# Performance work log

Measured on AMD Instinct MI355X. Metric: run time of the kernel, lower is better.

## Reference

```python
import jax, jax.numpy as jnp
import numpy as np

N_REL = 8


def setup_inputs() -> dict:
    key = jax.random.key(0)
    ks = jax.random.split(key, 16)
    N, E = 100_000, 1_600_000
    rn = lambda k, shape, s=0.1: jax.random.normal(k, shape, dtype=jnp.float32) * s
    return {
        "x": rn(ks[0], (N, 3), 1.0),
        "edge_index": jax.random.randint(ks[1], (2, E), 0, N),
        "edge_attr": rn(ks[2], (E, 2), 1.0),
        "edge_type": jax.random.randint(ks[3], (E,), 0, N_REL),
        "omega": rn(ks[4], (N, 2), 1.0),
        # encoder weights
        "Wn": rn(ks[5], (3, 64)), "bn": jnp.zeros((64,), jnp.float32),
        "We": rn(ks[6], (2, 32)), "be": jnp.zeros((32,), jnp.float32),
        "Wo": rn(ks[7], (2, 64)), "bo": jnp.zeros((64,), jnp.float32),
        # RGCN layer 1 (edge-feature-aware): per-relation W over concat(x_src, e) -> 64
        "W1": rn(ks[8], (N_REL, 96, 64)), "Wroot1": rn(ks[9], (64, 64)), "b1": jnp.zeros((64,), jnp.float32),
        # RGCN layer 2 (PyG RGCNConv, aggr='max')
        "W2": rn(ks[10], (N_REL, 64, 64)), "Wroot2": rn(ks[11], (64, 64)), "b2": jnp.zeros((64,), jnp.float32),
        # head
        "Wagg": rn(ks[12], (128, 64)), "bagg": jnp.zeros((64,), jnp.float32),
        "Wc": rn(ks[13], (64, 1)), "bc": jnp.zeros((1,), jnp.float32),
    }


def reference(x, edge_index, edge_attr, edge_type, omega,
              Wn, bn, We, be, Wo, bo,
              W1, Wroot1, b1, W2, Wroot2, b2,
              Wagg, bagg, Wc, bc):
    N = x.shape[0]
    n = jax.nn.relu(x @ Wn + bn)            # [N,64]
    e = jax.nn.relu(edge_attr @ We + be)    # [E,32]
    o = jax.nn.relu(omega @ Wo + bo)        # [N,64]
    src, dst = edge_index[0], edge_index[1]

    # --- RGCN layer 1: per-relation transform of [x_src || e], sum-aggregate ---
    feat = jnp.concatenate([n[src], e], axis=1)  # [E,96]
    acc = n @ Wroot1 + b1                        # root/self term
    for r in range(N_REL):
        m = (edge_type == r).astype(feat.dtype)[:, None]
        acc = acc + jax.ops.segment_sum((feat * m) @ W1[r], dst, num_segments=N)
    h = jax.nn.relu(acc)                         # [N,64]

    # --- RGCN layer 2: per-relation transform of x_src, max-aggregate per relation, sum over relations ---
    hs = h[src]                                  # [E,64]
    neg = jnp.finfo(h.dtype).min
    acc2 = h @ Wroot2 + b2
    for r in range(N_REL):
        mask = (edge_type == r)[:, None]
        msg = jnp.where(mask, hs @ W2[r], neg)
        mx = jax.ops.segment_max(msg, dst, num_segments=N)
        acc2 = acc2 + jnp.where(mx > neg * 0.5, mx, 0.0)  # empty segments -> 0 (PyG zeros-init scatter)
    h2 = jax.nn.relu(acc2)                       # [N,64]

    out = jax.nn.relu(jnp.concatenate([h2, o], axis=1) @ Wagg + bagg)
    return jnp.tanh(out @ Wc + bc) * 5.0
```

## Files before the change

### kernel.cpp

```cpp
#include <hip/hip_runtime.h>
#include <cmath>

typedef __attribute__((ext_vector_type(8))) short short8;
typedef __attribute__((ext_vector_type(4))) float floatx4;

__device__ __forceinline__ unsigned short rnbf(float f) {
    unsigned u = __float_as_uint(f);
    u += 0x7fffu + ((u >> 16) & 1u);
    return (unsigned short)(u >> 16);
}
__device__ __forceinline__ float bf2f(unsigned short h) {
    return __uint_as_float(((unsigned)h) << 16);
}
__device__ __forceinline__ int rfl(int v) { return __builtin_amdgcn_readfirstlane(v); }
__device__ __forceinline__ float eAct(unsigned ry, float we0, float we1, float bev) {
    float a0 = __uint_as_float(ry & 0xFFFF0000u);
    float a1 = __uint_as_float(ry << 16);
    return fmaxf(fmaf(a1, we1, fmaf(a0, we0, bev)), 0.f);
}
__device__ __forceinline__ unsigned vidx(int x, unsigned pl, int lane) {
    return (((unsigned)x >> 24) & 7u)*pl + (unsigned)(x & 0xFFFFFF)*64u + (unsigned)lane;
}
__device__ __forceinline__ void mstep(int r, float v, int& cur, float& mx, float& add) {
    bool nb = (r != cur);
    add += nb ? mx : 0.f;
    mx = nb ? v : fmaxf(mx, v);
    cur = r;
}

__global__ void k_histd(const int* __restrict__ ei, const int* __restrict__ et,
                        int* __restrict__ deg8, int E)
{
    int e = blockIdx.x*blockDim.x + threadIdx.x;
    if (e < E) atomicAdd(&deg8[ei[E + e]*8 + et[e]], 1);
}
#define SCHUNK 1024
__global__ void k_bsum(const int* __restrict__ deg, int* __restrict__ bsum, int K)
{
    __shared__ int s[256];
    int b = blockIdx.x, t = threadIdx.x;
    int base = b*SCHUNK;
    int v = 0;
    for (int k = t; k < SCHUNK; k += 256) { int i = base + k; v += (i < K) ? deg[i] : 0; }
    s[t] = v; __syncthreads();
    for (int o = 128; o; o >>= 1) { if (t < o) s[t] += s[t+o]; __syncthreads(); }
    if (t == 0) bsum[b] = s[0];
}
__global__ void k_bscan(int* __restrict__ bsum, int nb)
{
    __shared__ int ts[256];
    int t = threadIdx.x;
    int v[4]; int loc = 0;
    #pragma unroll
    for (int u = 0; u < 4; ++u) { int i = t*4+u; v[u] = (i < nb) ? bsum[i] : 0; loc += v[u]; }
    ts[t] = loc; __syncthreads();
    for (int o = 1; o < 256; o <<= 1) {
        int add = (t >= o) ? ts[t-o] : 0;
        __syncthreads();
        ts[t] += add;
        __syncthreads();
    }
    int excl = ts[t] - loc;
    #pragma unroll
    for (int u = 0; u < 4; ++u) {
        int i = t*4+u;
        if (i < nb) bsum[i] = excl;
        excl += v[u];
    }
}
__global__ void k_bapply(const int* __restrict__ deg, const int* __restrict__ bsum,
                         int* __restrict__ off, int* __restrict__ cursor, int K)
{
    __shared__ int ts[256];
    int b = blockIdx.x, t = threadIdx.x;
    int base = b*SCHUNK;
    int v[4]; int loc = 0;
    #pragma unroll
    for (int u = 0; u < 4; ++u) { int i = base + t*4 + u; v[u] = (i < K) ? deg[i] : 0; loc += v[u]; }
    ts[t] = loc; __syncthreads();
    for (int o = 1; o < 256; o <<= 1) {
        int add = (t >= o) ? ts[t-o] : 0;
        __syncthreads();
        ts[t] += add;
        __syncthreads();
    }
    int excl = ts[t] - loc + bsum[b];
    #pragma unroll
    for (int u = 0; u < 4; ++u) {
        int i = base + t*4 + u;
        if (i < K) { off[i] = excl; cursor[i] = excl; }
        excl += v[u];
        if (i == K-1) off[K] = excl;
    }
}
__global__ void k_scatd(const int* __restrict__ ei, const float* __restrict__ ea,
                        const int* __restrict__ et, int* __restrict__ cursor,
                        int2* __restrict__ srec, int E)
{
    int e = blockIdx.x*blockDim.x + threadIdx.x;
    if (e >= E) return;
    int rel = et[e];
    int key = ei[E + e]*8 + rel;
    int pos = atomicAdd(&cursor[key], 1);
    float2 a = ((const float2*)ea)[e];
    int xv = ei[e] | (rel << 24);
    int yv = ((int)rnbf(a.x) << 16) | (int)rnbf(a.y);
    srec[pos] = make_int2(xv, yv);
}

#define PB_KEYS 4096
#define PA_CH   4096
__global__ __launch_bounds__(256) void k_cnt256(
    const int* __restrict__ ei, int* __restrict__ bktCnt, int E, int nbkt)
{
    __shared__ int cnt[512];
    for (int j = threadIdx.x; j < nbkt; j += 256) cnt[j] = 0;
    __syncthreads();
    int stride = gridDim.x*256;
    for (int e = blockIdx.x*256 + threadIdx.x; e < E; e += stride)
        atomicAdd(&cnt[ei[E + e] >> 9], 1);
    __syncthreads();
    for (int j = threadIdx.x; j < nbkt; j += 256) {
        int c = cnt[j];
        if (c) atomicAdd(&bktCnt[j], c);
    }
}
__global__ void k_scan256(const int* __restrict__ bktCnt, int* __restrict__ bktBase,
                          int* __restrict__ bktCur, int nbkt)
{
    __shared__ int ts[256];
    int t = threadIdx.x;
    int v = (t < nbkt) ? bktCnt[t] : 0;
    ts[t] = v; __syncthreads();
    for (int o = 1; o < 256; o <<= 1) {
        int add = (t >= o) ? ts[t-o] : 0;
        __syncthreads();
        ts[t] += add;
        __syncthreads();
    }
    int excl = ts[t] - v;
    if (t < nbkt) { bktBase[t] = excl; bktCur[t] = excl; }
    if (t == nbkt - 1) bktBase[nbkt] = excl + v;
}
__global__ __launch_bounds__(256) void k_partA(
    const int* __restrict__ ei, const float* __restrict__ ea,
    const int* __restrict__ et, int* __restrict__ bktCur,
    int2* __restrict__ tmp, int E, int nbkt)
{
    __shared__ int cnt[512], base[512];
    int b0 = blockIdx.x * PA_CH;
    for (int j = threadIdx.x; j < nbkt; j += 256) cnt[j] = 0;
    __syncthreads();
    int2 rec[16]; int bk[16];
    #pragma unroll
    for (int u = 0; u < 16; ++u) {
        int e = b0 + u*256 + threadIdx.x;
        bk[u] = -1;
        if (e < E) {
            int rel = et[e];
            int src = ei[e];
            int dst = ei[E + e];
            float2 a = ((const float2*)ea)[e];
            rec[u] = make_int2(src | (rel << 17) | ((dst & 511) << 20),
                               ((int)rnbf(a.x) << 16) | (int)rnbf(a.y));
            bk[u] = dst >> 9;
            atomicAdd(&cnt[bk[u]], 1);
        }
    }
    __syncthreads();
    for (int j = threadIdx.x; j < nbkt; j += 256) {
        int c = cnt[j];
        base[j] = c ? atomicAdd(&bktCur[j], c) : 0;
    }
    __syncthreads();
    for (int j = threadIdx.x; j < nbkt; j += 256) cnt[j] = 0;
    __syncthreads();
    #pragma unroll
    for (int u = 0; u < 16; ++u) {
        if (bk[u] >= 0) {
            int pos = base[bk[u]] + atomicAdd(&cnt[bk[u]], 1);
            tmp[pos] = rec[u];
        }
    }
}
__global__ __launch_bounds__(256) void k_partB2(
    const int2* __restrict__ tmp, const int* __restrict__ bktBase,
    int* __restrict__ off8, int2* __restrict__ srec, int K8)
{
    __shared__ int cnt[PB_KEYS];
    __shared__ int ts[256];
    int b = blockIdx.x;
    int kbase = b * PB_KEYS;
    int kend = kbase + PB_KEYS; if (kend > K8) kend = K8;
    int nk = kend - kbase;
    int bstart = bktBase[b];
    int bend = bktBase[b + 1];
    int t = threadIdx.x;
    for (int j = t; j < PB_KEYS; j += 256) cnt[j] = 0;
    __syncthreads();
    for (int i = bstart + t; i < bend; i += 256) {
        unsigned xw = (unsigned)tmp[i].x;
        int key = (int)((xw >> 20) & 511u)*8 + (int)((xw >> 17) & 7u);
        atomicAdd(&cnt[key], 1);
    }
    __syncthreads();
    int loc[16]; int lsum = 0;
    #pragma unroll
    for (int u = 0; u < 16; ++u) { loc[u] = cnt[t*16 + u]; lsum += loc[u]; }
    ts[t] = lsum; __syncthreads();
    for (int o = 1; o < 256; o <<= 1) {
        int add = (t >= o) ? ts[t-o] : 0;
        __syncthreads();
        ts[t] += add;
        __syncthreads();
    }
    int excl = ts[t] - lsum + bstart;
    #pragma unroll
    for (int u = 0; u < 16; ++u) {
        int j = t*16 + u;
        cnt[j] = excl;
        if (j < nk) off8[kbase + j] = excl;
        excl += loc[u];
    }
    if (t == 0 && kend == K8) off8[K8] = bend;
    __syncthreads();
    for (int i = bstart + t; i < bend; i += 256) {
        int2 r = tmp[i];
        unsigned xw = (unsigned)r.x;
        int src = (int)(xw & 0x1FFFFu);
        int rel = (int)((xw >> 17) & 7u);
        int key = (int)((xw >> 20) & 511u)*8 + rel;
        int pos = atomicAdd(&cnt[key], 1);
        srec[pos] = make_int2(src | (rel << 24), r.y);
    }
}

__global__ __launch_bounds__(64) void k_wpack(
    const float* __restrict__ W1, const float* __restrict__ W2,
    const float* __restrict__ Wroot1, const float* __restrict__ Wroot2,
    const float* __restrict__ Wagg, unsigned short* __restrict__ wpk)
{
    int unit = blockIdx.x >> 2;
    int jt = blockIdx.x & 3;
    int lane = threadIdx.x;
    const float* Wb;
    int kbase;
    if (unit < 16) {
        Wb = W1 + (size_t)(unit >> 1)*96*64;
        kbase = (unit & 1)*32;
    } else if (unit < 32) {
        Wb = W2 + (size_t)((unit - 16) >> 1)*64*64;
        kbase = ((unit - 16) & 1)*32;
    } else if (unit < 40) {
        Wb = W1 + (size_t)(unit - 32)*96*64;
        kbase = 64;
    } else if (unit < 42) {
        Wb = Wroot1; kbase = (unit - 40)*32;
    } else if (unit < 44) {
        Wb = Wroot2; kbase = (unit - 42)*32;
    } else {
        Wb = Wagg;   kbase = (unit - 44)*32;
    }
    int j = jt*16 + (lane & 15);
    size_t base = (((size_t)unit*4 + jt)*64 + lane)*16;
    #pragma unroll
    for (int i = 0; i < 8; ++i) {
        int k = kbase + (lane >> 4)*8 + i;
        float f = Wb[(size_t)k*64 + j];
        unsigned short hi = rnbf(f);
        unsigned short lo = rnbf(f - bf2f(hi));
        wpk[base + i] = hi;
        wpk[base + 8 + i] = lo;
    }
}

__global__ __launch_bounds__(256) void k_encV(
    const float* __restrict__ x,
    const float* __restrict__ Wn, const float* __restrict__ bn,
    const unsigned short* __restrict__ wpk, const float* __restrict__ b1,
    float* __restrict__ acc1, unsigned short* __restrict__ Vbf,
    size_t plane, int N)
{
    int lane = threadIdx.x & 63;
    int wave = threadIdx.x >> 6;
    int n0 = blockIdx.x*64 + 16*wave;
    int m = lane & 15, q = lane >> 4;
    int node = n0 + m; if (node >= N) node = N - 1;
    float x0 = x[3*node], x1 = x[3*node+1], x2 = x[3*node+2];
    short8 ah[2], al[2];
    #pragma unroll
    for (int ks = 0; ks < 2; ++ks) {
        #pragma unroll
        for (int i = 0; i < 8; ++i) {
            int f = ks*32 + q*8 + i;
            float nf = fmaxf(fmaf(x2, Wn[128+f], fmaf(x1, Wn[64+f], fmaf(x0, Wn[f], bn[f]))), 0.f);
            unsigned short hb = rnbf(nf);
            ah[ks][i] = (short)hb;
            al[ks][i] = (short)rnbf(nf - bf2f(hb));
        }
    }
    {
        floatx4 acc[4];
        #pragma unroll
        for (int jt = 0; jt < 4; ++jt) acc[jt] = (floatx4){0.f,0.f,0.f,0.f};
        #pragma unroll
        for (int ks = 0; ks < 2; ++ks) {
            int unit = 40 + ks;
            #pragma unroll
            for (int jt = 0; jt < 4; ++jt) {
                const unsigned short* qp = wpk + (((size_t)unit*4 + jt)*64 + lane)*16;
                short8 bh = *(const short8*)qp;
                short8 bl = *(const short8*)(qp + 8);
                acc[jt] = __builtin_amdgcn_mfma_f32_16x16x32_bf16(ah[ks], bh, acc[jt], 0,0,0);
                acc[jt] = __builtin_amdgcn_mfma_f32_16x16x32_bf16(ah[ks], bl, acc[jt], 0,0,0);
                acc[jt] = __builtin_amdgcn_mfma_f32_16x16x32_bf16(al[ks], bh, acc[jt], 0,0,0);
            }
        }
        #pragma unroll
        for (int jt = 0; jt < 4; ++jt) {
            float bb = b1[jt*16 + m];
            #pragma unroll
            for (int t = 0; t < 4; ++t) {
                int row = n0 + q*4 + t;
                if (row < N) acc1[(size_t)row*64 + jt*16 + m] = acc[jt][t] + bb;
            }
        }
    }
    for (int p = 0; p < 8; ++p) {
        floatx4 acc[4];
        #pragma unroll
        for (int jt = 0; jt < 4; ++jt) acc[jt] = (floatx4){0.f,0.f,0.f,0.f};
        #pragma unroll
        for (int ks = 0; ks < 2; ++ks) {
            int unit = p*2 + ks;
            #pragma unroll
            for (int jt = 0; jt < 4; ++jt) {
                const unsigned short* qp = wpk + (((size_t)unit*4 + jt)*64 + lane)*16;
                short8 bh = *(const short8*)qp;
                short8 bl = *(const short8*)(qp + 8);
                acc[jt] = __builtin_amdgcn_mfma_f32_16x16x32_bf16(ah[ks], bh, acc[jt], 0,0,0);
                acc[jt] = __builtin_amdgcn_mfma_f32_16x16x32_bf16(ah[ks], bl, acc[jt], 0,0,0);
                acc[jt] = __builtin_amdgcn_mfma_f32_16x16x32_bf16(al[ks], bh, acc[jt], 0,0,0);
            }
        }
        unsigned short* Vp = Vbf + (size_t)p*plane;
        #pragma unroll
        for (int jt = 0; jt < 4; ++jt) {
            #pragma unroll
            for (int t = 0; t < 4; ++t) {
                int row = n0 + q*4 + t;
                if (row < N) Vp[(size_t)row*64 + jt*16 + m] = rnbf(acc[jt][t]);
            }
        }
    }
}

__global__ __launch_bounds__(256) void k_encB(
    const float* __restrict__ x,
    const float* __restrict__ Wn, const float* __restrict__ bn,
    const unsigned short* __restrict__ wpk, const float* __restrict__ b1,
    float* __restrict__ nbuf, float* __restrict__ acc1, int N)
{
    int lane = threadIdx.x & 63;
    int wave = threadIdx.x >> 6;
    int n0 = blockIdx.x*64 + 16*wave;
    int m = lane & 15, q = lane >> 4;
    #pragma unroll 4
    for (int t = 0; t < 16; ++t) {
        int nd = n0 + t;
        if (nd < N) {
            float x0 = x[3*nd], x1 = x[3*nd+1], x2 = x[3*nd+2];
            float nj = fmaxf(fmaf(x2, Wn[128+lane], fmaf(x1, Wn[64+lane], fmaf(x0, Wn[lane], bn[lane]))), 0.f);
            nbuf[(size_t)nd*64 + lane] = nj;
        }
    }
    int node = n0 + m; if (node >= N) node = N - 1;
    float x0 = x[3*node], x1 = x[3*node+1], x2 = x[3*node+2];
    short8 ah[2], al[2];
    #pragma unroll
    for (int ks = 0; ks < 2; ++ks) {
        #pragma unroll
        for (int i = 0; i < 8; ++i) {
            int f = ks*32 + q*8 + i;
            float nf = fmaxf(fmaf(x2, Wn[128+f], fmaf(x1, Wn[64+f], fmaf(x0, Wn[f], bn[f]))), 0.f);
            unsigned short hb = rnbf(nf);
            ah[ks][i] = (short)hb;
            al[ks][i] = (short)rnbf(nf - bf2f(hb));
        }
    }
    floatx4 acc[4];
    #pragma unroll
    for (int jt = 0; jt < 4; ++jt) acc[jt] = (floatx4){0.f,0.f,0.f,0.f};
    #pragma unroll
    for (int ks = 0; ks < 2; ++ks) {
        int unit = 40 + ks;
        #pragma unroll
        for (int jt = 0; jt < 4; ++jt) {
            const unsigned short* qp = wpk + (((size_t)unit*4 + jt)*64 + lane)*16;
            short8 bh = *(const short8*)qp;
            short8 bl = *(const short8*)(qp + 8);
            acc[jt] = __builtin_amdgcn_mfma_f32_16x16x32_bf16(ah[ks], bh, acc[jt], 0,0,0);
            acc[jt] = __builtin_amdgcn_mfma_f32_16x16x32_bf16(ah[ks], bl, acc[jt], 0,0,0);
            acc[jt] = __builtin_amdgcn_mfma_f32_16x16x32_bf16(al[ks], bh, acc[jt], 0,0,0);
        }
    }
    #pragma unroll
    for (int jt = 0; jt < 4; ++jt) {
        float bb = b1[jt*16 + m];
        #pragma unroll
        for (int t = 0; t < 4; ++t) {
            int row = n0 + q*4 + t;
            if (row < N) acc1[(size_t)row*64 + jt*16 + m] = acc[jt][t] + bb;
        }
    }
}

__global__ __launch_bounds__(256) void k_vgemmB(
    const float* __restrict__ F, const unsigned short* __restrict__ wpk,
    int unitBase, int g0, int Gc, unsigned short* __restrict__ Vbf,
    size_t plane, int N)
{
    int lane = threadIdx.x & 63;
    int wave = threadIdx.x >> 6;
    int n0 = blockIdx.x*64 + 16*wave;
    int m = lane & 15, q = lane >> 4;
    int node = n0 + m;
    if (node >= N) node = N - 1;
    const float4* Fr = (const float4*)(F + (size_t)node*64);
    short8 ah[2], al[2];
    #pragma unroll
    for (int ks = 0; ks < 2; ++ks) {
        float4 u0 = Fr[ks*8 + q*2];
        float4 u1 = Fr[ks*8 + q*2 + 1];
        float fv[8] = {u0.x,u0.y,u0.z,u0.w,u1.x,u1.y,u1.z,u1.w};
        #pragma unroll
        for (int i = 0; i < 8; ++i) {
            unsigned short hb = rnbf(fv[i]);
            ah[ks][i] = (short)hb;
            al[ks][i] = (short)rnbf(fv[i] - bf2f(hb));
        }
    }
    for (int p = 0; p < Gc; ++p) {
        int rel = g0 + p;
        floatx4 acc[4];
        #pragma unroll
        for (int jt = 0; jt < 4; ++jt) acc[jt] = (floatx4){0.f,0.f,0.f,0.f};
        #pragma unroll
        for (int ks = 0; ks < 2; ++ks) {
            int unit = unitBase + rel*2 + ks;
            #pragma unroll
            for (int jt = 0; jt < 4; ++jt) {
                const unsigned short* qp = wpk + (((size_t)unit*4 + jt)*64 + lane)*16;
                short8 bh = *(const short8*)qp;
                short8 bl = *(const short8*)(qp + 8);
                acc[jt] = __builtin_amdgcn_mfma_f32_16x16x32_bf16(ah[ks], bh, acc[jt], 0,0,0);
                acc[jt] = __builtin_amdgcn_mfma_f32_16x16x32_bf16(ah[ks], bl, acc[jt], 0,0,0);
                acc[jt] = __builtin_amdgcn_mfma_f32_16x16x32_bf16(al[ks], bh, acc[jt], 0,0,0);
            }
        }
        unsigned short* Vp = Vbf + (size_t)p*plane;
        #pragma unroll
        for (int jt = 0; jt < 4; ++jt) {
            #pragma unroll
            for (int t = 0; t < 4; ++t) {
                int row = n0 + q*4 + t;
                if (row < N) Vp[(size_t)row*64 + jt*16 + m] = rnbf(acc[jt][t]);
            }
        }
    }
}

__global__ __launch_bounds__(256) void k_agg1ef(
    const int2* __restrict__ srec, const int* __restrict__ off8,
    const unsigned short* __restrict__ Vbf, size_t plane,
    const float* __restrict__ We, const float* __restrict__ be,
    float* __restrict__ acc1, unsigned short* __restrict__ Sep, int N)
{
    int lane = threadIdx.x & 63;
    int wv = threadIdx.x >> 6;
    unsigned pl = (unsigned)plane;
    float we0 = We[lane & 31], we1 = We[32 + (lane & 31)], bev = be[lane & 31];
    int stride = gridDim.x*4;
    for (int node = blockIdx.x*4 + wv; node < N; node += stride) {
        const int* ofp = off8 + node*8;
        int o0 = rfl(ofp[0]), o8 = rfl(ofp[8]);
        float vsum = 0.f;
        int i = o0;
        for (; i + 16 <= o8; i += 16) {
            int2 q[16];
            #pragma unroll
            for (int u = 0; u < 16; ++u) q[u] = srec[i+u];
            int xs[16];
            #pragma unroll
            for (int u = 0; u < 16; ++u) xs[u] = rfl(q[u].x);
            float v[16];
            #pragma unroll
            for (int u = 0; u < 16; ++u) v[u] = bf2f(Vbf[vidx(xs[u], pl, lane)]);
            float s01 = (v[0]+v[1]) + (v[2]+v[3]);
            float s23 = (v[4]+v[5]) + (v[6]+v[7]);
            float s45 = (v[8]+v[9]) + (v[10]+v[11]);
            float s67 = (v[12]+v[13]) + (v[14]+v[15]);
            vsum += (s01 + s23) + (s45 + s67);
        }
        for (; i + 8 <= o8; i += 8) {
            int2 q0 = srec[i+0], q1 = srec[i+1], q2 = srec[i+2], q3 = srec[i+3];
            int2 q4 = srec[i+4], q5 = srec[i+5], q6 = srec[i+6], q7 = srec[i+7];
// ... 420 lines not shown
    int lane = threadIdx.x & 63;
    int wv = threadIdx.x >> 6;
    int stride = gridDim.x*4;
    const float NEG = -__builtin_inff();
    for (int node = blockIdx.x*4 + wv; node < N; node += stride) {
        float add = 0.f;
        bool any = false;
        for (int r = g0; r < g1; ++r) {
            int s = rfl(off8[node*8 + r]);
            int e = rfl(off8[node*8 + r + 1]);
            if (s == e) continue;
            any = true;
            const unsigned short* Up = Ubf + (size_t)(r - g0)*plane;
            float mx = NEG;
            int i = s;
            for (; i + 8 <= e; i += 8) {
                int s0 = rfl(srec[i+0].x) & 0xFFFFFF, s1 = rfl(srec[i+1].x) & 0xFFFFFF;
                int s2 = rfl(srec[i+2].x) & 0xFFFFFF, s3 = rfl(srec[i+3].x) & 0xFFFFFF;
                int s4 = rfl(srec[i+4].x) & 0xFFFFFF, s5 = rfl(srec[i+5].x) & 0xFFFFFF;
                int s6 = rfl(srec[i+6].x) & 0xFFFFFF, s7 = rfl(srec[i+7].x) & 0xFFFFFF;
                float v0 = bf2f(Up[(size_t)s0*64 + lane]), v1 = bf2f(Up[(size_t)s1*64 + lane]);
                float v2 = bf2f(Up[(size_t)s2*64 + lane]), v3 = bf2f(Up[(size_t)s3*64 + lane]);
                float v4 = bf2f(Up[(size_t)s4*64 + lane]), v5 = bf2f(Up[(size_t)s5*64 + lane]);
                float v6 = bf2f(Up[(size_t)s6*64 + lane]), v7 = bf2f(Up[(size_t)s7*64 + lane]);
                float m01 = fmaxf(v0, v1), m23 = fmaxf(v2, v3);
                float m45 = fmaxf(v4, v5), m67 = fmaxf(v6, v7);
                mx = fmaxf(mx, fmaxf(fmaxf(m01, m23), fmaxf(m45, m67)));
            }
            for (; i < e; ++i) {
                int sx = rfl(srec[i].x) & 0xFFFFFF;
                mx = fmaxf(mx, bf2f(Up[(size_t)sx*64 + lane]));
            }
            add += mx;
        }
        if (any) acc2[(size_t)node*64 + lane] += add;
    }
}

__global__ __launch_bounds__(256) void k_finB(
    const float* __restrict__ acc2, const float* __restrict__ omega,
    const float* __restrict__ Wo, const float* __restrict__ bo,
    const unsigned short* __restrict__ wpk,
    const float* __restrict__ bagg, const float* __restrict__ Wc,
    const float* __restrict__ bc, float* __restrict__ out, int N)
{
    int lane = threadIdx.x & 63;
    int wave = threadIdx.x >> 6;
    int n0 = blockIdx.x*64 + 16*wave;
    int m = lane & 15, q = lane >> 4;
    int node = n0 + m;
    if (node >= N) node = N - 1;
    short8 ah[4], al[4];
    const float4* Fr = (const float4*)(acc2 + (size_t)node*64);
    #pragma unroll
    for (int ks = 0; ks < 2; ++ks) {
        float4 u0 = Fr[ks*8 + q*2];
        float4 u1 = Fr[ks*8 + q*2 + 1];
        float fv[8] = {u0.x,u0.y,u0.z,u0.w,u1.x,u1.y,u1.z,u1.w};
        #pragma unroll
        for (int i = 0; i < 8; ++i) {
            float hv = fmaxf(fv[i], 0.f);
            unsigned short hb = rnbf(hv);
            ah[ks][i] = (short)hb;
            al[ks][i] = (short)rnbf(hv - bf2f(hb));
        }
    }
    float om0 = omega[2*node], om1 = omega[2*node+1];
    #pragma unroll
    for (int ks = 2; ks < 4; ++ks) {
        #pragma unroll
        for (int i = 0; i < 8; ++i) {
            int f = (ks - 2)*32 + q*8 + i;
            float ov = fmaxf(fmaf(om1, Wo[64+f], fmaf(om0, Wo[f], bo[f])), 0.f);
            unsigned short hb = rnbf(ov);
            ah[ks][i] = (short)hb;
            al[ks][i] = (short)rnbf(ov - bf2f(hb));
        }
    }
    floatx4 acc[4];
    #pragma unroll
    for (int jt = 0; jt < 4; ++jt) acc[jt] = (floatx4){0.f,0.f,0.f,0.f};
    #pragma unroll
    for (int ks = 0; ks < 4; ++ks) {
        int unit = 44 + ks;
        #pragma unroll
        for (int jt = 0; jt < 4; ++jt) {
            const unsigned short* qp = wpk + (((size_t)unit*4 + jt)*64 + lane)*16;
            short8 bh = *(const short8*)qp;
            short8 bl = *(const short8*)(qp + 8);
            acc[jt] = __builtin_amdgcn_mfma_f32_16x16x32_bf16(ah[ks], bh, acc[jt], 0,0,0);
            acc[jt] = __builtin_amdgcn_mfma_f32_16x16x32_bf16(ah[ks], bl, acc[jt], 0,0,0);
            acc[jt] = __builtin_amdgcn_mfma_f32_16x16x32_bf16(al[ks], bh, acc[jt], 0,0,0);
        }
    }
    float bg0 = bagg[m], bg1 = bagg[16+m], bg2 = bagg[32+m], bg3 = bagg[48+m];
    float wc0 = Wc[m],   wc1 = Wc[16+m],   wc2 = Wc[32+m],   wc3 = Wc[48+m];
    float bc0 = bc[0];
    #pragma unroll
    for (int t = 0; t < 4; ++t) {
        float s = fmaxf(acc[0][t] + bg0, 0.f)*wc0
                + fmaxf(acc[1][t] + bg1, 0.f)*wc1
                + fmaxf(acc[2][t] + bg2, 0.f)*wc2
                + fmaxf(acc[3][t] + bg3, 0.f)*wc3;
        s += __shfl_xor(s, 1);
        s += __shfl_xor(s, 2);
        s += __shfl_xor(s, 4);
        s += __shfl_xor(s, 8);
        int row = n0 + q*4 + t;
        if (m == 0 && row < N) out[row] = tanhf(s + bc0) * 5.0f;
    }
}

extern "C" void kernel_launch(void* const* d_in, const int* in_sizes, int n_in,
                              void* d_out, int out_size, void* d_ws, size_t ws_size,
                              hipStream_t stream)
{
    const float* x      = (const float*)d_in[0];
    const int*   ei     = (const int*)d_in[1];
    const float* ea     = (const float*)d_in[2];
    const int*   et     = (const int*)d_in[3];
    const float* omega  = (const float*)d_in[4];
    const float* Wn     = (const float*)d_in[5];
    const float* bn     = (const float*)d_in[6];
    const float* We     = (const float*)d_in[7];
    const float* be     = (const float*)d_in[8];
    const float* Wo     = (const float*)d_in[9];
    const float* bo     = (const float*)d_in[10];
    const float* W1     = (const float*)d_in[11];
    const float* Wroot1 = (const float*)d_in[12];
    const float* b1     = (const float*)d_in[13];
    const float* W2     = (const float*)d_in[14];
    const float* Wroot2 = (const float*)d_in[15];
    const float* b2     = (const float*)d_in[16];
    const float* Wagg   = (const float*)d_in[17];
    const float* bagg   = (const float*)d_in[18];
    const float* Wc     = (const float*)d_in[19];
    const float* bc     = (const float*)d_in[20];
    int N = in_sizes[0] / 3;
    int E = in_sizes[3];
    float* out = (float*)d_out;

    int K8 = N*8;
    int nb = (K8 + SCHUNK - 1)/SCHUNK;

    #define ALIGN256(p) ((char*)(((size_t)(p) + 255) & ~(size_t)255))
    char* pp = (char*)d_ws;
    float* nbuf   = (float*)pp;  pp = ALIGN256(pp + (size_t)N*64*4);
    float* acc1   = (float*)pp;  pp = ALIGN256(pp + (size_t)N*64*4);
    int2*  srec   = (int2*)pp;   pp = ALIGN256(pp + (size_t)E*8);
    int*   deg8   = (int*)pp;    pp = ALIGN256(pp + (size_t)K8*4);
    int*   off8   = (int*)pp;    pp = ALIGN256(pp + (size_t)(K8+1)*4);
    int*   cursor = (int*)pp;    pp = ALIGN256(pp + (size_t)K8*4);
    int*   bsum   = (int*)pp;    pp = ALIGN256(pp + (size_t)nb*4);
    int*   bktCur = (int*)pp;    pp = ALIGN256(pp + (size_t)512*4);
    int*   bktBase= (int*)pp;    pp = ALIGN256(pp + (size_t)520*4);
    unsigned short* wpk = (unsigned short*)pp;
    pp = ALIGN256(pp + (size_t)48*4*64*16*2);
    unsigned short* Sepool = (unsigned short*)pp;
    pp = ALIGN256(pp + (size_t)N*256*2);
    size_t off = (size_t)(pp - (char*)d_ws);
    size_t planeElems = (size_t)N*64;
    size_t avail = (ws_size > off) ? (ws_size - off) : 0;
    int G = (int)(avail / (planeElems*2));
    if (G > 8) G = 8;
    if (G < 1) G = 1;
    unsigned short* Vbf = (unsigned short*)pp;
    float* acc2 = nbuf;

    int gblocks = (N + 63)/64;
    int nbkt = (N + 511) >> 9;
    bool fastSort = (N <= 131072) && ((size_t)E*8 <= (size_t)N*256*2);

    k_wpack<<<192, 64, 0, stream>>>(W1, W2, Wroot1, Wroot2, Wagg, wpk);
    if (G == 8) {
        k_encV<<<gblocks, 256, 0, stream>>>(x, Wn, bn, wpk, b1, acc1, Vbf, planeElems, N);
    } else {
        k_encB<<<gblocks, 256, 0, stream>>>(x, Wn, bn, wpk, b1, nbuf, acc1, N);
    }

    if (fastSort) {
        int2* tmp = (int2*)Sepool;
        hipMemsetAsync(deg8, 0, (size_t)nbkt*4, stream);
        k_cnt256<<<1024, 256, 0, stream>>>(ei, deg8, E, nbkt);
        k_scan256<<<1, 256, 0, stream>>>(deg8, bktBase, bktCur, nbkt);
        k_partA<<<(E + PA_CH - 1)/PA_CH, 256, 0, stream>>>(ei, ea, et, bktCur, tmp, E, nbkt);
        k_partB2<<<nbkt, 256, 0, stream>>>(tmp, bktBase, off8, srec, K8);
    } else {
        hipMemsetAsync(deg8, 0, (size_t)K8*4, stream);
        k_histd<<<(E + 255)/256, 256, 0, stream>>>(ei, et, deg8, E);
        k_bsum<<<nb, 256, 0, stream>>>(deg8, bsum, K8);
        k_bscan<<<1, 256, 0, stream>>>(bsum, nb);
        k_bapply<<<nb, 256, 0, stream>>>(deg8, bsum, off8, cursor, K8);
        k_scatd<<<(E + 255)/256, 256, 0, stream>>>(ei, ea, et, cursor, srec, E);
    }

    int aggBlocks = 4096;
    if (G == 8) {
        k_agg1ef<<<aggBlocks, 256, 0, stream>>>(srec, off8, Vbf, planeElems, We, be,
                                                acc1, Sepool, N);
        k_seghrowV<<<gblocks, 256, 0, stream>>>(Sepool, wpk, acc1, acc2, b2,
                                                Vbf, planeElems, N);
        k_agg2f<<<aggBlocks, 256, 0, stream>>>(srec, off8, Vbf, planeElems, acc2, N);
    } else {
        int Gc1 = G;
        k_vgemmB<<<gblocks, 256, 0, stream>>>(nbuf, wpk, 0, 0, Gc1, Vbf, planeElems, N);
        k_agg1e<<<aggBlocks, 256, 0, stream>>>(srec, off8, Vbf, planeElems, We, be,
                                               acc1, Sepool, N, Gc1);
        for (int g0 = Gc1; g0 < 8; g0 += G) {
            int Gc = (8 - g0 < G) ? (8 - g0) : G;
            k_vgemmB<<<gblocks, 256, 0, stream>>>(nbuf, wpk, 0, g0, Gc, Vbf, planeElems, N);
            k_agg1v<<<aggBlocks, 256, 0, stream>>>(srec, off8, Vbf, planeElems,
                                                   acc1, N, g0, g0 + Gc);
        }
        k_segemm<<<gblocks, 256, 0, stream>>>(Sepool, wpk, acc1, N);
        k_hrowB<<<gblocks, 256, 0, stream>>>(acc1, acc2, wpk, b2, N);
        for (int g0 = 0; g0 < 8; g0 += G) {
            int Gc = (8 - g0 < G) ? (8 - g0) : G;
            k_vgemmB<<<gblocks, 256, 0, stream>>>(acc1, wpk, 16, g0, Gc, Vbf, planeElems, N);
            k_agg2<<<aggBlocks, 256, 0, stream>>>(srec, off8, Vbf, planeElems,
                                                  acc2, N, g0, g0 + Gc);
        }
    }
    k_finB<<<gblocks, 256, 0, stream>>>(acc2, omega, Wo, bo, wpk, bagg, Wc, bc, out, N);
}
```

Measured before the change: 469.4 us.

## Fuse encoder and bucket count into one launch, fold scans into partition kernels

Merges the node encoder/V-plane GEMM kernel and the destination-bucket histogram into a single launch that splits work by block index. The standalone single-block scan kernel is removed, and each partition kernel recomputes the small bucket prefix sum itself, with a separate relative cursor array. The aim is fewer kernel launches and serialization points in the sort pipeline. In exchange, every partition block repeats a 256-wide scan.

```diff
diff --git a/kernel.cpp b/kernel.cpp
--- a/kernel.cpp
+++ b/kernel.cpp
@@ -110,14 +110,17 @@
 
 #define PB_KEYS 4096
 #define PA_CH   4096
-__global__ __launch_bounds__(256) void k_cnt256(
-    const int* __restrict__ ei, int* __restrict__ bktCnt, int E, int nbkt)
+#define CNTB    512
+
+__device__ __forceinline__ void dev_cnt(const int* __restrict__ ei,
+                                        int* __restrict__ bktCnt,
+                                        int E, int nbkt, int cb, int cgrid)
 {
     __shared__ int cnt[512];
     for (int j = threadIdx.x; j < nbkt; j += 256) cnt[j] = 0;
     __syncthreads();
-    int stride = gridDim.x*256;
-    for (int e = blockIdx.x*256 + threadIdx.x; e < E; e += stride)
+    int stride = cgrid*256;
+    for (int e = cb*256 + threadIdx.x; e < E; e += stride)
         atomicAdd(&cnt[ei[E + e] >> 9], 1);
     __syncthreads();
     for (int j = threadIdx.x; j < nbkt; j += 256) {
@@ -125,36 +128,131 @@
         if (c) atomicAdd(&bktCnt[j], c);
     }
 }
-__global__ void k_scan256(const int* __restrict__ bktCnt, int* __restrict__ bktBase,
-                          int* __restrict__ bktCur, int nbkt)
-{
+
+__device__ __forceinline__ void dev_encV(
+    const float* __restrict__ x,
+    const float* __restrict__ Wn, const float* __restrict__ bn,
+    const unsigned short* __restrict__ wpk, const float* __restrict__ b1,
+    float* __restrict__ acc1, unsigned short* __restrict__ Vbf,
+    size_t plane, int N, int bid)
+{
+    int lane = threadIdx.x & 63;
+    int wave = threadIdx.x >> 6;
+    int n0 = bid*64 + 16*wave;
+    int m = lane & 15, q = lane >> 4;
+    int node = n0 + m; if (node >= N) node = N - 1;
+    float x0 = x[3*node], x1 = x[3*node+1], x2 = x[3*node+2];
+    short8 ah[2], al[2];
+    #pragma unroll
+    for (int ks = 0; ks < 2; ++ks) {
+        #pragma unroll
+        for (int i = 0; i < 8; ++i) {
+            int f = ks*32 + q*8 + i;
+            float nf = fmaxf(fmaf(x2, Wn[128+f], fmaf(x1, Wn[64+f], fmaf(x0, Wn[f], bn[f]))), 0.f);
+            unsigned short hb = rnbf(nf);
+            ah[ks][i] = (short)hb;
+            al[ks][i] = (short)rnbf(nf - bf2f(hb));
+        }
+    }
+    {
+        floatx4 acc[4];
+        #pragma unroll
+        for (int jt = 0; jt < 4; ++jt) acc[jt] = (floatx4){0.f,0.f,0.f,0.f};
+        #pragma unroll
+        for (int ks = 0; ks < 2; ++ks) {
+            int unit = 40 + ks;
+            #pragma unroll
+            for (int jt = 0; jt < 4; ++jt) {
+                const unsigned short* qp = wpk + (((size_t)unit*4 + jt)*64 + lane)*16;
+                short8 bh = *(const short8*)qp;
+                short8 bl = *(const short8*)(qp + 8);
+                acc[jt] = __builtin_amdgcn_mfma_f32_16x16x32_bf16(ah[ks], bh, acc[jt], 0,0,0);
+                acc[jt] = __builtin_amdgcn_mfma_f32_16x16x32_bf16(ah[ks], bl, acc[jt], 0,0,0);
+                acc[jt] = __builtin_amdgcn_mfma_f32_16x16x32_bf16(al[ks], bh, acc[jt], 0,0,0);
+            }
+        }
+        #pragma unroll
+        for (int jt = 0; jt < 4; ++jt) {
+            float bb = b1[jt*16 + m];
+            #pragma unroll
+            for (int t = 0; t < 4; ++t) {
+                int row = n0 + q*4 + t;
+                if (row < N) acc1[(size_t)row*64 + jt*16 + m] = acc[jt][t] + bb;
+            }
+        }
+    }
+    for (int p = 0; p < 8; ++p) {
+        floatx4 acc[4];
+        #pragma unroll
+        for (int jt = 0; jt < 4; ++jt) acc[jt] = (floatx4){0.f,0.f,0.f,0.f};
+        #pragma unroll
+        for (int ks = 0; ks < 2; ++ks) {
+            int unit = p*2 + ks;
+            #pragma unroll
+            for (int jt = 0; jt < 4; ++jt) {
+                const unsigned short* qp = wpk + (((size_t)unit*4 + jt)*64 + lane)*16;
+                short8 bh = *(const short8*)qp;
+                short8 bl = *(const short8*)(qp + 8);
+                acc[jt] = __builtin_amdgcn_mfma_f32_16x16x32_bf16(ah[ks], bh, acc[jt], 0,0,0);
+                acc[jt] = __builtin_amdgcn_mfma_f32_16x16x32_bf16(ah[ks], bl, acc[jt], 0,0,0);
+                acc[jt] = __builtin_amdgcn_mfma_f32_16x16x32_bf16(al[ks], bh, acc[jt], 0,0,0);
+            }
+        }
+        unsigned short* Vp = Vbf + (size_t)p*plane;
+        #pragma unroll
+        for (int jt = 0; jt < 4; ++jt) {
+            #pragma unroll
+            for (int t = 0; t < 4; ++t) {
+                int row = n0 + q*4 + t;
+                if (row < N) Vp[(size_t)row*64 + jt*16 + m] = rnbf(acc[jt][t]);
+            }
+        }
+    }
+}
+
+__global__ __launch_bounds__(256) void k_phase1(
+    const float* __restrict__ x,
+    const float* __restrict__ Wn, const float* __restrict__ bn,
+    const unsigned short* __restrict__ wpk, const float* __restrict__ b1,
+    float* __restrict__ acc1, unsigned short* __restrict__ Vbf,
+    size_t plane, int N,
+    const int* __restrict__ ei, int* __restrict__ bktCnt, int E, int nbkt,
+    int encBlocks, int cntBlocks)
+{
+    int bid = (int)blockIdx.x;
+    if (bid < encBlocks) {
+        dev_encV(x, Wn, bn, wpk, b1, acc1, Vbf, plane, N, bid);
+    } else {
+        dev_cnt(ei, bktCnt, E, nbkt, bid - encBlocks, cntBlocks);
+    }
+}
+
+__global__ __launch_bounds__(256) void k_partA(
+    const int* __restrict__ ei, const float* __restrict__ ea,
+    const int* __restrict__ et, const int* __restrict__ bktCnt,
+    int* __restrict__ cursorRel, int2* __restrict__ tmp, int E, int nbkt)
+{
+    __shared__ int cnt[512], base[512], gbase[256];
     __shared__ int ts[256];
     int t = threadIdx.x;
-    int v = (t < nbkt) ? bktCnt[t] : 0;
-    ts[t] = v; __syncthreads();
-    for (int o = 1; o < 256; o <<= 1) {
-        int add = (t >= o) ? ts[t-o] : 0;
-        __syncthreads();
-        ts[t] += add;
-        __syncthreads();
-    }
-    int excl = ts[t] - v;
-    if (t < nbkt) { bktBase[t] = excl; bktCur[t] = excl; }
-    if (t == nbkt - 1) bktBase[nbkt] = excl + v;
-}
-__global__ __launch_bounds__(256) void k_partA(
-    const int* __restrict__ ei, const float* __restrict__ ea,
-    const int* __restrict__ et, int* __restrict__ bktCur,
-    int2* __restrict__ tmp, int E, int nbkt)
-{
-    __shared__ int cnt[512], base[512];
+    {
+        int v = (t < nbkt) ? bktCnt[t] : 0;
+        ts[t] = v; __syncthreads();
+        for (int o = 1; o < 256; o <<= 1) {
+            int add = (t >= o) ? ts[t-o] : 0;
+            __syncthreads();
+            ts[t] += add;
+            __syncthreads();
+        }
+        gbase[t] = ts[t] - v;
+    }
     int b0 = blockIdx.x * PA_CH;
-    for (int j = threadIdx.x; j < nbkt; j += 256) cnt[j] = 0;
+    for (int j = t; j < nbkt; j += 256) cnt[j] = 0;
     __syncthreads();
     int2 rec[16]; int bk[16];
     #pragma unroll
     for (int u = 0; u < 16; ++u) {
-        int e = b0 + u*256 + threadIdx.x;
+        int e = b0 + u*256 + t;
         bk[u] = -1;
         if (e < E) {
             int rel = et[e];
@@ -168,12 +266,12 @@
         }
     }
     __syncthreads();
-    for (int j = threadIdx.x; j < nbkt; j += 256) {
+    for (int j = t; j < nbkt; j += 256) {
         int c = cnt[j];
-        base[j] = c ? atomicAdd(&bktCur[j], c) : 0;
+        base[j] = c ? (gbase[j] + atomicAdd(&cursorRel[j], c)) : 0;
     }
     __syncthreads();
-    for (int j = threadIdx.x; j < nbkt; j += 256) cnt[j] = 0;
+    for (int j = t; j < nbkt; j += 256) cnt[j] = 0;
     __syncthreads();
     #pragma unroll
     for (int u = 0; u < 16; ++u) {
@@ -184,18 +282,31 @@
     }
 }
 __global__ __launch_bounds__(256) void k_partB2(
-    const int2* __restrict__ tmp, const int* __restrict__ bktBase,
-    int* __restrict__ off8, int2* __restrict__ srec, int K8)
+    const int2* __restrict__ tmp, const int* __restrict__ bktCnt,
+    int* __restrict__ off8, int2* __restrict__ srec, int K8, int nbkt)
 {
     __shared__ int cnt[PB_KEYS];
     __shared__ int ts[256];
+    __shared__ int sb[2];
     int b = blockIdx.x;
+    int t = threadIdx.x;
+    {
+        int v = (t < nbkt) ? bktCnt[t] : 0;
+        ts[t] = v; __syncthreads();
+        for (int o = 1; o < 256; o <<= 1) {
+            int add = (t >= o) ? ts[t-o] : 0;
+            __syncthreads();
+            ts[t] += add;
+            __syncthreads();
+        }
+        if (t == b) { sb[0] = ts[t] - v; sb[1] = ts[t]; }
+    }
+    __syncthreads();
+    int bstart = sb[0];
+    int bend = sb[1];
     int kbase = b * PB_KEYS;
     int kend = kbase + PB_KEYS; if (kend > K8) kend = K8;
     int nk = kend - kbase;
-    int bstart = bktBase[b];
-    int bend = bktBase[b + 1];
-    int t = threadIdx.x;
     for (int j = t; j < PB_KEYS; j += 256) cnt[j] = 0;
     __syncthreads();
     for (int i = bstart + t; i < bend; i += 256) {
@@ -271,87 +382,6 @@
         unsigned short lo = rnbf(f - bf2f(hi));
         wpk[base + i] = hi;
         wpk[base + 8 + i] = lo;
-    }
-}
-
-__global__ __launch_bounds__(256) void k_encV(
-    const float* __restrict__ x,
-    const float* __restrict__ Wn, const float* __restrict__ bn,
-    const unsigned short* __restrict__ wpk, const float* __restrict__ b1,
-    float* __restrict__ acc1, unsigned short* __restrict__ Vbf,
-    size_t plane, int N)
-{
-    int lane = threadIdx.x & 63;
-    int wave = threadIdx.x >> 6;
-    int n0 = blockIdx.x*64 + 16*wave;
-    int m = lane & 15, q = lane >> 4;
-    int node = n0 + m; if (node >= N) node = N - 1;
-    float x0 = x[3*node], x1 = x[3*node+1], x2 = x[3*node+2];
-    short8 ah[2], al[2];
-    #pragma unroll
-    for (int ks = 0; ks < 2; ++ks) {
-        #pragma unroll
-        for (int i = 0; i < 8; ++i) {
-            int f = ks*32 + q*8 + i;
-            float nf = fmaxf(fmaf(x2, Wn[128+f], fmaf(x1, Wn[64+f], fmaf(x0, Wn[f], bn[f]))), 0.f);
-            unsigned short hb = rnbf(nf);
-            ah[ks][i] = (short)hb;
-            al[ks][i] = (short)rnbf(nf - bf2f(hb));
-        }
-    }
-    {
-        floatx4 acc[4];
-        #pragma unroll
-        for (int jt = 0; jt < 4; ++jt) acc[jt] = (floatx4){0.f,0.f,0.f,0.f};
-        #pragma unroll
-        for (int ks = 0; ks < 2; ++ks) {
-            int unit = 40 + ks;
-            #pragma unroll
-            for (int jt = 0; jt < 4; ++jt) {
-                const unsigned short* qp = wpk + (((size_t)unit*4 + jt)*64 + lane)*16;
-                short8 bh = *(const short8*)qp;
-                short8 bl = *(const short8*)(qp + 8);
-                acc[jt] = __builtin_amdgcn_mfma_f32_16x16x32_bf16(ah[ks], bh, acc[jt], 0,0,0);
-                acc[jt] = __builtin_amdgcn_mfma_f32_16x16x32_bf16(ah[ks], bl, acc[jt], 0,0,0);
-                acc[jt] = __builtin_amdgcn_mfma_f32_16x16x32_bf16(al[ks], bh, acc[jt], 0,0,0);
-            }
-        }
-        #pragma unroll
-        for (int jt = 0; jt < 4; ++jt) {
-            float bb = b1[jt*16 + m];
-            #pragma unroll
-            for (int t = 0; t < 4; ++t) {
-                int row = n0 + q*4 + t;
-                if (row < N) acc1[(size_t)row*64 + jt*16 + m] = acc[jt][t] + bb;
-            }
-        }
-    }
-    for (int p = 0; p < 8; ++p) {
-        floatx4 acc[4];
-        #pragma unroll
-        for (int jt = 0; jt < 4; ++jt) acc[jt] = (floatx4){0.f,0.f,0.f,0.f};
-        #pragma unroll
-        for (int ks = 0; ks < 2; ++ks) {
-            int unit = p*2 + ks;
-            #pragma unroll
-            for (int jt = 0; jt < 4; ++jt) {
-                const unsigned short* qp = wpk + (((size_t)unit*4 + jt)*64 + lane)*16;
-                short8 bh = *(const short8*)qp;
-                short8 bl = *(const short8*)(qp + 8);
-                acc[jt] = __builtin_amdgcn_mfma_f32_16x16x32_bf16(ah[ks], bh, acc[jt], 0,0,0);
-                acc[jt] = __builtin_amdgcn_mfma_f32_16x16x32_bf16(ah[ks], bl, acc[jt], 0,0,0);
-                acc[jt] = __builtin_amdgcn_mfma_f32_16x16x32_bf16(al[ks], bh, acc[jt], 0,0,0);
-            }
-        }
-        unsigned short* Vp = Vbf + (size_t)p*plane;
-        #pragma unroll
-        for (int jt = 0; jt < 4; ++jt) {
-            #pragma unroll
-            for (int t = 0; t < 4; ++t) {
-                int row = n0 + q*4 + t;
-                if (row < N) Vp[(size_t)row*64 + jt*16 + m] = rnbf(acc[jt][t]);
-            }
-        }
     }
 }
 
@@ -1078,8 +1108,6 @@
     int*   off8   = (int*)pp;    pp = ALIGN256(pp + (size_t)(K8+1)*4);
     int*   cursor = (int*)pp;    pp = ALIGN256(pp + (size_t)K8*4);
     int*   bsum   = (int*)pp;    pp = ALIGN256(pp + (size_t)nb*4);
-    int*   bktCur = (int*)pp;    pp = ALIGN256(pp + (size_t)512*4);
-    int*   bktBase= (int*)pp;    pp = ALIGN256(pp + (size_t)520*4);
     unsigned short* wpk = (unsigned short*)pp;
     pp = ALIGN256(pp + (size_t)48*4*64*16*2);
     unsigned short* Sepool = (unsigned short*)pp;
@@ -1096,23 +1124,35 @@
     int gblocks = (N + 63)/64;
     int nbkt = (N + 511) >> 9;
     bool fastSort = (N <= 131072) && ((size_t)E*8 <= (size_t)N*256*2);
-
+    int* bktCnt = deg8;
+    int* cursorRel = deg8 + 512;
+
+    if (fastSort) hipMemsetAsync(deg8, 0, 4096, stream);
+    else          hipMemsetAsync(deg8, 0, (size_t)K8*4, stream);
     k_wpack<<<192, 64, 0, stream>>>(W1, W2, Wroot1, Wroot2, Wagg, wpk);
-    if (G == 8) {
-        k_encV<<<gblocks, 256, 0, stream>>>(x, Wn, bn, wpk, b1, acc1, Vbf, planeElems, N);
+
+    if (G == 8 && fastSort) {
+        k_phase1<<<gblocks + CNTB, 256, 0, stream>>>(x, Wn, bn, wpk, b1, acc1, Vbf,
+                                                     planeElems, N, ei, bktCnt, E, nbkt,
+                                                     gblocks, CNTB);
+    } else if (G == 8) {
+        k_phase1<<<gblocks, 256, 0, stream>>>(x, Wn, bn, wpk, b1, acc1, Vbf,
+                                              planeElems, N, ei, bktCnt, E, nbkt,
+                                              gblocks, 0);
     } else {
         k_encB<<<gblocks, 256, 0, stream>>>(x, Wn, bn, wpk, b1, nbuf, acc1, N);
+        if (fastSort)
+            k_phase1<<<CNTB, 256, 0, stream>>>(x, Wn, bn, wpk, b1, acc1, Vbf,
+                                               planeElems, N, ei, bktCnt, E, nbkt,
+                                               0, CNTB);
     }
 
     if (fastSort) {
         int2* tmp = (int2*)Sepool;
-        hipMemsetAsync(deg8, 0, (size_t)nbkt*4, stream);
-        k_cnt256<<<1024, 256, 0, stream>>>(ei, deg8, E, nbkt);
-        k_scan256<<<1, 256, 0, stream>>>(deg8, bktBase, bktCur, nbkt);
-        k_partA<<<(E + PA_CH - 1)/PA_CH, 256, 0, stream>>>(ei, ea, et, bktCur, tmp, E, nbkt);
-        k_partB2<<<nbkt, 256, 0, stream>>>(tmp, bktBase, off8, srec, K8);
+        k_partA<<<(E + PA_CH - 1)/PA_CH, 256, 0, stream>>>(ei, ea, et, bktCnt,
+                                                           cursorRel, tmp, E, nbkt);
+        k_partB2<<<nbkt, 256, 0, stream>>>(tmp, bktCnt, off8, srec, K8, nbkt);
     } else {
-        hipMemsetAsync(deg8, 0, (size_t)K8*4, stream);
         k_histd<<<(E + 255)/256, 256, 0, stream>>>(ei, et, deg8, E);
         k_bsum<<<nb, 256, 0, stream>>>(deg8, bsum, K8);
         k_bscan<<<1, 256, 0, stream>>>(bsum, nb);
```

Result: faster. 452.3 us (median of 2 runs) (-3.6%).
